# Kernel optimization log

Measured on AMD Instinct MI355X. Metric: run time of the kernel, lower is better.

## Reference

```python
import jax, jax.numpy as jnp
import numpy as np

C_IN = 512
OUT_CH = 256  # query/key gate channels
DIM = 64      # squeeze/extraction rank


def setup_inputs() -> dict:
    key = jax.random.key(0)
    ks = jax.random.split(key, 11)
    b, c, h, w = 16, C_IN, 64, 64

    def winit(k, o, i):
        # torch Conv2d default init: U(-s, s), s = 1/sqrt(fan_in)
        s = 1.0 / np.sqrt(i)
        return jax.random.uniform(k, (o, i), jnp.float32, -s, s)

    return {
        "x": jax.random.normal(ks[0], (b, c, h, w), jnp.float32),
        "Wq": winit(ks[1], OUT_CH, C_IN), "bq": winit(ks[2], OUT_CH, C_IN)[:, 0],
        "Wk": winit(ks[3], OUT_CH, C_IN), "bk": winit(ks[4], OUT_CH, C_IN)[:, 0],
        "Wv": winit(ks[5], C_IN, C_IN),   "bv": winit(ks[6], C_IN, C_IN)[:, 0],
        "Ws": winit(ks[7], DIM, C_IN),    "bs": winit(ks[8], DIM, C_IN)[:, 0],
        "We": winit(ks[9], DIM, C_IN),    "be": winit(ks[10], DIM, C_IN)[:, 0],
    }


def reference(x, Wq, bq, Wk, bk, Wv, bv, Ws, bs, We, be):
    b, c, h, w = x.shape
    n = h * w
    xf = x.reshape(b, c, n)  # [b, 512, n] (1x1 conv == matmul over channels)

    Q = jnp.einsum('oc,bcn->bon', Wq, xf) + bq[:, None]   # [b, 256, n]
    K = jnp.einsum('oc,bcn->bon', Wk, xf) + bk[:, None]   # [b, 256, n]
    gate = jax.nn.sigmoid(jnp.mean(Q * K, axis=1, keepdims=True))  # [b, 1, n]

    V = jnp.einsum('oc,bcn->bon', Wv, xf) + bv[:, None]   # [b, 512, n]
    V_dw = V * gate                                        # [b, 512, n]

    Qs = jnp.einsum('oc,bcn->bon', Ws, xf) + bs[:, None]   # [b, 64, n]
    Ke = jnp.einsum('oc,bcn->bon', We, xf) + be[:, None]   # [b, 64, n]

    energy = jnp.einsum('bcn,bdn->bcd', V_dw, Qs)           # [b, 512, 64]
    attention = jax.nn.softmax(energy, axis=-1)
    Vout = jnp.einsum('bcd,bdn->bcn', attention, Ke)        # [b, 512, n]

    return x + Vout.reshape(b, c, h, w)
```

## Files before the change

### kernel.cpp

```cpp
#include <hip/hip_runtime.h>

#define BATCH 16
#define CIN 512
#define NPIX 4096

typedef __attribute__((ext_vector_type(8))) short bf16x8;
typedef __attribute__((ext_vector_type(4))) float f32x4;

#define MFMA(a,b,c) __builtin_amdgcn_mfma_f32_16x16x32_bf16((a),(b),(c),0,0,0)

union PK  { short s[8]; bf16x8 v; };
union PK4 { short s[4]; uint2 u; };

__device__ __forceinline__ unsigned short bf16_rne(float f){
  unsigned u = __float_as_uint(f);
  return (unsigned short)((u + 0x7fffu + ((u >> 16) & 1u)) >> 16);
}
__device__ __forceinline__ void f32_split(float f, short &h, short &l){
  unsigned short hu = bf16_rne(f);
  h = (short)hu;
  float fh = __uint_as_float((unsigned)hu << 16);
  l = (short)bf16_rne(f - fh);
}
__device__ __forceinline__ void split8(float4 a, float4 b, bf16x8 &h, bf16x8 &l){
  float vv[8] = {a.x,a.y,a.z,a.w,b.x,b.y,b.z,b.w};
  PK ph, pl;
  #pragma unroll
  for (int z=0;z<8;z++){ short hh,ll; f32_split(vv[z],hh,ll); ph.s[z]=hh; pl.s[z]=ll; }
  h = ph.v; l = pl.v;
}

__device__ __forceinline__ int offBig(int row, int k){
  int s = k >> 3;
  s = (s & ~7) | ((s ^ row) & 7);
  return row*512 + s*8 + (k & 7);
}

__global__ __launch_bounds__(256)
void k_convw(const float* __restrict__ Wq, const float* __restrict__ bq,
             const float* __restrict__ Wk, const float* __restrict__ bk,
             const float* __restrict__ Ws, const float* __restrict__ bs,
             const float* __restrict__ We, const float* __restrict__ be,
             short* __restrict__ WG, short* __restrict__ WSE, short* __restrict__ WSL,
             float* __restrict__ BG, float* __restrict__ BSE){
  int t = blockIdx.x*256 + threadIdx.x;
  if (t < 512*512){
    int r = t >> 9, c = t & 511, o = r >> 1;
    float v = (r & 1) ? Wk[o*512+c] : Wq[o*512+c];
    WG[t] = (short)bf16_rne(v);
  }
  if (t < 128*512){
    int r = t >> 9, c = t & 511;
    float v = (r < 64) ? Ws[r*512+c] : We[(r-64)*512+c];
    short h,l; f32_split(v,h,l);
    WSE[t] = h;
    if (r < 64) WSL[t] = l;
  }
  if (t < 512) BG[t] = (t&1) ? bk[t>>1] : bq[t>>1];
  if (t < 128) BSE[t] = (t < 64) ? bs[t] : be[t-64];
}

__global__ __launch_bounds__(512)
void k_front(const float* __restrict__ x, const short* __restrict__ WG,
             const float* __restrict__ BG, const short* __restrict__ WSE,
             const short* __restrict__ WSL, const float* __restrict__ BSE,
             float* __restrict__ QSG, short* __restrict__ KET, float* __restrict__ S){
  __shared__ __align__(16) short XS[64*512];
  __shared__ float QKf[512];
  __shared__ float GF[64];
  int nt = blockIdx.x, b = blockIdx.y;
  int n0 = nt*64;
  int tid = threadIdx.x, w = tid>>6, lane = tid&63;
  int lr = lane&15, lk = (lane>>4)<<3;
  bool isQs = (w < 4);
  const short* wgb = WG  + (size_t)(w*64 + lr)*512 + lk;
  const short* wb  = WSE + (size_t)((isQs ? (w*16) : (64 + (w-4)*16)) + lr)*512 + lk;
  const short* wlb = WSL + (size_t)((isQs ? (w*16) : 0) + lr)*512 + lk;

  {
    const float* xp = x + ((size_t)b*CIN + tid)*NPIX + n0;
    for (int i=0;i<64;i+=4){
      float4 v = *(const float4*)(xp + i);
      float vv[4] = {v.x, v.y, v.z, v.w};
      #pragma unroll
      for (int u=0;u<4;u++)
        XS[offBig(i+u, tid)] = (short)bf16_rne(vv[u]);
    }
  }
  __syncthreads();

  f32x4 acc1[4][4] = {};
  f32x4 acc2[4] = {};

  bf16x8 c0 = *(const bf16x8*)(wgb + 0*16*512);
  bf16x8 c1 = *(const bf16x8*)(wgb + 1*16*512);
  bf16x8 c2 = *(const bf16x8*)(wgb + 2*16*512);
  bf16x8 c3 = *(const bf16x8*)(wgb + 3*16*512);
  bf16x8 chh = *(const bf16x8*)(wb);
  bf16x8 cll = isQs ? *(const bf16x8*)(wlb) : chh;

  for (int kt=0; kt<16; kt++){
    bf16x8 n0f=c0, n1f=c1, n2f=c2, n3f=c3, nhf=chh, nlf=cll;
    if (kt < 15){
      int o = (kt+1)*32;
      n0f = *(const bf16x8*)(wgb + 0*16*512 + o);
      n1f = *(const bf16x8*)(wgb + 1*16*512 + o);
      n2f = *(const bf16x8*)(wgb + 2*16*512 + o);
      n3f = *(const bf16x8*)(wgb + 3*16*512 + o);
      nhf = *(const bf16x8*)(wb + o);
      nlf = isQs ? *(const bf16x8*)(wlb + o) : nhf;
    }
    bf16x8 bb[4];
    #pragma unroll
    for (int j=0;j<4;j++)
      bb[j] = *(const bf16x8*)&XS[offBig(j*16+lr, kt*32+lk)];
    if (isQs){
      #pragma unroll
      for (int j=0;j<4;j++){
        acc2[j] = MFMA(cll, bb[j], acc2[j]);
        acc2[j] = MFMA(chh, bb[j], acc2[j]);
      }
    } else {
      #pragma unroll
      for (int j=0;j<4;j++)
        acc2[j] = MFMA(chh, bb[j], acc2[j]);
    }
    #pragma unroll
    for (int j=0;j<4;j++) acc1[0][j] = MFMA(c0, bb[j], acc1[0][j]);
    #pragma unroll
    for (int j=0;j<4;j++) acc1[1][j] = MFMA(c1, bb[j], acc1[1][j]);
    #pragma unroll
    for (int j=0;j<4;j++) acc1[2][j] = MFMA(c2, bb[j], acc1[2][j]);
    #pragma unroll
    for (int j=0;j<4;j++) acc1[3][j] = MFMA(c3, bb[j], acc1[3][j]);
    c0=n0f; c1=n1f; c2=n2f; c3=n3f; chh=nhf; cll=nlf;
  }

  int rq = (lane>>4)<<2;
  {
    float p[4] = {0.f,0.f,0.f,0.f};
    #pragma unroll
    for (int r=0;r<4;r++){
      f32x4 bg = *(const f32x4*)&BG[w*64 + r*16 + rq];
      #pragma unroll
      for (int j=0;j<4;j++){
        f32x4 a4 = acc1[r][j];
        p[j] += (a4[0]+bg[0])*(a4[1]+bg[1]) + (a4[2]+bg[2])*(a4[3]+bg[3]);
      }
    }
    #pragma unroll
    for (int j=0;j<4;j++){ p[j] += __shfl_xor(p[j],16); p[j] += __shfl_xor(p[j],32); }
    if (lane < 16){
      #pragma unroll
      for (int j=0;j<4;j++) QKf[w*64 + j*16 + lane] = p[j];
    }
  }
  __syncthreads();
  if (tid < 64){
    float s = 0.f;
    #pragma unroll
    for (int ww=0;ww<8;ww++) s += QKf[ww*64 + tid];
    GF[tid] = 1.f/(1.f + __expf(-s*(1.f/256.f)));
  }
  __syncthreads();

  if (isQs){
    int row0 = w*16 + rq;
    f32x4 bs4 = *(const f32x4*)&BSE[row0];
    float srow[4] = {0.f,0.f,0.f,0.f};
    #pragma unroll
    for (int j=0;j<4;j++){
      int nl = j*16 + lr;
      float g = GF[nl];
      int n = n0 + nl;
      #pragma unroll
      for (int q=0;q<4;q++){
        float v = (acc2[j][q] + bs4[q]) * g;
        QSG[((size_t)(b*64) + row0 + q)*NPIX + n] = v;
        srow[q] += v;
      }
    }
    #pragma unroll
    for (int q=0;q<4;q++){
      float v = srow[q];
      v += __shfl_xor(v,1); v += __shfl_xor(v,2);
      v += __shfl_xor(v,4); v += __shfl_xor(v,8);
      if (lr == 0) atomicAdd(&S[b*64 + row0 + q], v);
    }
  } else {
    int d0 = (w-4)*16 + rq;
    f32x4 be4 = *(const f32x4*)&BSE[64 + d0];
    #pragma unroll
    for (int j=0;j<4;j++){
      int n = n0 + j*16 + lr;
      PK4 pk;
      #pragma unroll
      for (int q=0;q<4;q++) pk.s[q] = (short)bf16_rne(acc2[j][q] + be4[q]);
      *(uint2*)&KET[((size_t)(b*NPIX) + n)*64 + d0] = pk.u;
    }
  }
}

__global__ __launch_bounds__(512)
void k_M(const float* __restrict__ x, const float* __restrict__ QSG,
         float* __restrict__ M){
  int slab = blockIdx.x, b = blockIdx.y;
  int tid = threadIdx.x, w = tid>>6, lane = tid&63;
  int lr = lane&15, lk8 = (lane>>4)<<3;
  f32x4 acc[4][4] = {};
  for (int kt=0; kt<4; kt++){
    int noff = slab*128 + kt*32 + lk8;
    bf16x8 bh[4], bl[4];
    #pragma unroll
    for (int j=0;j<4;j++){
      const float* qp = QSG + ((size_t)(b*64) + j*16 + lr)*NPIX + noff;
      split8(*(const float4*)qp, *(const float4*)(qp+4), bh[j], bl[j]);
    }
    #pragma unroll
    for (int r=0;r<4;r++){
      const float* xp = x + ((size_t)(b*CIN) + w*64 + r*16 + lr)*NPIX + noff;
      bf16x8 ah, al;
      split8(*(const float4*)xp, *(const float4*)(xp+4), ah, al);
      #pragma unroll
      for (int j=0;j<4;j++){
        acc[r][j] = MFMA(al, bh[j], acc[r][j]);
        acc[r][j] = MFMA(ah, bl[j], acc[r][j]);
        acc[r][j] = MFMA(ah, bh[j], acc[r][j]);
      }
    }
  }
  int rq = (lane>>4)<<2;
  #pragma unroll
  for (int r=0;r<4;r++)
    #pragma unroll
    for (int j=0;j<4;j++)
      #pragma unroll
      for (int q=0;q<4;q++)
        atomicAdd(&M[((size_t)(b*CIN) + w*64 + r*16 + rq + q)*64 + j*16 + lr], acc[r][j][q]);
}

__global__ __launch_bounds__(256)
void k_energy(const float* __restrict__ Wv, const float* __restrict__ bv,
              const float* __restrict__ M, const float* __restrict__ S,
              float* __restrict__ EN){
  __shared__ __align__(16) float ML[128*68];
  int cch = blockIdx.x, b = blockIdx.y;
  int tid = threadIdx.x;
  int d4 = tid & 15, ci = tid >> 4;
  f32x4 acc[2] = {};
  for (int kt=0; kt<4; kt++){
    __syncthreads();
    for (int i = tid; i < 2048; i += 256){
      int k = i >> 4, c4 = (i & 15) * 4;
      *(float4*)&ML[k*68 + c4] = *(const float4*)&M[((size_t)(b*CIN) + kt*128 + k)*64 + c4];
    }
    __syncthreads();
    #pragma unroll
    for (int m=0;m<2;m++){
      int c = cch*32 + ci + 16*m;
      const float* wvp = Wv + (size_t)c*512 + kt*128;
      for (int k4=0;k4<32;k4++){
        float4 wv4 = *(const float4*)(wvp + k4*4);
        f32x4 m0 = *(const f32x4*)&ML[(k4*4+0)*68 + d4*4];
        f32x4 m1 = *(const f32x4*)&ML[(k4*4+1)*68 + d4*4];
        f32x4 m2 = *(const f32x4*)&ML[(k4*4+2)*68 + d4*4];
        f32x4 m3 = *(const f32x4*)&ML[(k4*4+3)*68 + d4*4];
        acc[m] += m0*wv4.x + m1*wv4.y + m2*wv4.z + m3*wv4.w;
      }
    }
  }
  f32x4 s4 = *(const f32x4*)&S[b*64 + d4*4];
  #pragma unroll
  for (int m=0;m<2;m++){
    int c = cch*32 + ci + 16*m;
    f32x4 r = acc[m] + s4*bv[c];
    *(f32x4*)&EN[((size_t)(b*CIN) + c)*64 + d4*4] = r;
  }
}

__global__ __launch_bounds__(256)
void k_softmax(const float* __restrict__ EN, short* __restrict__ ATT){
  int row = blockIdx.x*4 + (threadIdx.x>>6);
  int lane = threadIdx.x & 63;
  float v = EN[(size_t)row*64 + lane];
  float m = v;
  #pragma unroll
  for (int s=1;s<64;s<<=1) m = fmaxf(m, __shfl_xor(m, s));
  float e = __expf(v - m);
  float sum = e;
  #pragma unroll
  for (int s=1;s<64;s<<=1) sum += __shfl_xor(sum, s);
  ATT[(size_t)row*64 + lane] = (short)bf16_rne(e / sum);
}

__global__ __launch_bounds__(512)
void k_out(const float* __restrict__ x, const short* __restrict__ ATT,
           const short* __restrict__ KET, float* __restrict__ out){
  int nt = blockIdx.x, b = blockIdx.y;
  int n0 = nt*64;
  int tid = threadIdx.x, w = tid>>6, lane = tid&63;
  int lr = lane&15, lk = (lane>>4)<<3;
  f32x4 acc[4][4] = {};
  #pragma unroll
  for (int kt=0; kt<2; kt++){
    bf16x8 bb[4];
    #pragma unroll
    for (int j=0;j<4;j++)
      bb[j] = *(const bf16x8*)&KET[((size_t)(b*NPIX) + n0 + j*16 + lr)*64 + kt*32 + lk];
    #pragma unroll
    for (int r=0;r<4;r++){
      bf16x8 a = *(const bf16x8*)&ATT[((size_t)(b*CIN) + w*64 + r*16 + lr)*64 + kt*32 + lk];
      #pragma unroll
      for (int j=0;j<4;j++)
        acc[r][j] = MFMA(a, bb[j], acc[r][j]);
    }
  }
  int rq = (lane>>4)<<2;
  #pragma unroll
  for (int r=0;r<4;r++)
    #pragma unroll
    for (int j=0;j<4;j++){
      int col = n0 + j*16 + lr;
      #pragma unroll
      for (int q=0;q<4;q++){
        size_t idx = ((size_t)(b*CIN) + w*64 + r*16 + rq + q)*NPIX + col;
        out[idx] = x[idx] + acc[r][j][q];
      }
    }
}

extern "C" void kernel_launch(void* const* d_in, const int* in_sizes, int n_in,
                              void* d_out, int out_size, void* d_ws, size_t ws_size,
                              hipStream_t stream){
  const float* x   = (const float*)d_in[0];
  const float* Wq  = (const float*)d_in[1];
  const float* bq  = (const float*)d_in[2];
  const float* Wk  = (const float*)d_in[3];
  const float* bk  = (const float*)d_in[4];
  const float* Wv  = (const float*)d_in[5];
  const float* bv  = (const float*)d_in[6];
  const float* Wsq = (const float*)d_in[7];
  const float* bsq = (const float*)d_in[8];
  const float* We  = (const float*)d_in[9];
  const float* be  = (const float*)d_in[10];
  float* out = (float*)d_out;

  char* wsb = (char*)d_ws;
  size_t off = 0;
  auto alloc = [&](size_t bytes)->void*{
    void* p = wsb + off; off += (bytes + 255) & ~(size_t)255; return p;
  };
  short* WG   = (short*)alloc((size_t)512*512*2);
  short* WSE  = (short*)alloc((size_t)128*512*2);
  short* WSL  = (short*)alloc((size_t)64*512*2);
  float* BG   = (float*)alloc(512*4);
  float* BSE  = (float*)alloc(128*4);
  float* QSG  = (float*)alloc((size_t)BATCH*64*NPIX*4);
  short* KET  = (short*)alloc((size_t)BATCH*NPIX*64*2);
  float* Mb   = (float*)alloc((size_t)BATCH*512*64*4);
  float* Sb   = (float*)alloc((size_t)BATCH*64*4);
  float* EN   = (float*)alloc((size_t)BATCH*512*64*4);
  short* ATT  = (short*)alloc((size_t)BATCH*512*64*2);

  hipMemsetAsync(Mb, 0, (size_t)BATCH*512*64*4, stream);
  hipMemsetAsync(Sb, 0, (size_t)BATCH*64*4, stream);

  k_convw  <<<1024, 256, 0, stream>>>(Wq,bq,Wk,bk,Wsq,bsq,We,be, WG,WSE,WSL,BG,BSE);
  k_front  <<<dim3(64,16), 512, 0, stream>>>(x, WG, BG, WSE, WSL, BSE, QSG, KET, Sb);
  k_M      <<<dim3(32,16), 512, 0, stream>>>(x, QSG, Mb);
  k_energy <<<dim3(16,16), 256, 0, stream>>>(Wv, bv, Mb, Sb, EN);
  k_softmax<<<2048, 256, 0, stream>>>(EN, ATT);
  k_out    <<<dim3(64,16), 512, 0, stream>>>(x, ATT, KET, out);
}
```

Measured before the change: 305.4 us.

## Widen k_front to 128-pixel tiles with 1024 threads; double k_M slab

k_front now runs 1024-thread blocks covering 128 pixels, with two 8-wave groups sharing one LDS tile of x and the same weight rows, halving the grid. k_M processes 256 pixels per slab instead of 128, halving its grid and its atomic/partial outputs. The aim is better amortisation of weight loads and fewer blocks, at the cost of 128 KB of LDS per block, lower occupancy, and fewer blocks to fill the CUs (512 and 256 blocks).

```diff
diff --git a/kernel.cpp b/kernel.cpp
--- a/kernel.cpp
+++ b/kernel.cpp
@@ -60,31 +60,34 @@
   if (t < 128) BSE[t] = (t < 64) ? bs[t] : be[t-64];
 }
 
-__global__ __launch_bounds__(512)
+__global__ __launch_bounds__(1024)
 void k_front(const float* __restrict__ x, const short* __restrict__ WG,
              const float* __restrict__ BG, const short* __restrict__ WSE,
              const short* __restrict__ WSL, const float* __restrict__ BSE,
              float* __restrict__ QSG, short* __restrict__ KET, float* __restrict__ S){
-  __shared__ __align__(16) short XS[64*512];
-  __shared__ float QKf[512];
-  __shared__ float GF[64];
+  __shared__ __align__(16) short XS[128*512];
+  __shared__ float QKf[1024];
+  __shared__ float GF[128];
   int nt = blockIdx.x, b = blockIdx.y;
-  int n0 = nt*64;
+  int n0 = nt*128;
   int tid = threadIdx.x, w = tid>>6, lane = tid&63;
+  int wl = w & 7, wg = w >> 3;
+  int n0g = n0 + wg*64;
   int lr = lane&15, lk = (lane>>4)<<3;
-  bool isQs = (w < 4);
-  const short* wgb = WG  + (size_t)(w*64 + lr)*512 + lk;
-  const short* wb  = WSE + (size_t)((isQs ? (w*16) : (64 + (w-4)*16)) + lr)*512 + lk;
-  const short* wlb = WSL + (size_t)((isQs ? (w*16) : 0) + lr)*512 + lk;
+  bool isQs = (wl < 4);
+  const short* wgb = WG  + (size_t)(wl*64 + lr)*512 + lk;
+  const short* wb  = WSE + (size_t)((isQs ? (wl*16) : (64 + (wl-4)*16)) + lr)*512 + lk;
+  const short* wlb = WSL + (size_t)((isQs ? (wl*16) : 0) + lr)*512 + lk;
 
   {
-    const float* xp = x + ((size_t)b*CIN + tid)*NPIX + n0;
+    int cl = tid & 511, nh = tid >> 9;
+    const float* xp = x + ((size_t)b*CIN + cl)*NPIX + n0 + nh*64;
     for (int i=0;i<64;i+=4){
       float4 v = *(const float4*)(xp + i);
       float vv[4] = {v.x, v.y, v.z, v.w};
       #pragma unroll
       for (int u=0;u<4;u++)
-        XS[offBig(i+u, tid)] = (short)bf16_rne(vv[u]);
+        XS[offBig(nh*64 + i+u, cl)] = (short)bf16_rne(vv[u]);
     }
   }
   __syncthreads();
@@ -113,7 +116,7 @@
     bf16x8 bb[4];
     #pragma unroll
     for (int j=0;j<4;j++)
-      bb[j] = *(const bf16x8*)&XS[offBig(j*16+lr, kt*32+lk)];
+      bb[j] = *(const bf16x8*)&XS[offBig(wg*64 + j*16 + lr, kt*32 + lk)];
     if (isQs){
       #pragma unroll
       for (int j=0;j<4;j++){
@@ -141,7 +144,7 @@
     float p[4] = {0.f,0.f,0.f,0.f};
     #pragma unroll
     for (int r=0;r<4;r++){
-      f32x4 bg = *(const f32x4*)&BG[w*64 + r*16 + rq];
+      f32x4 bg = *(const f32x4*)&BG[wl*64 + r*16 + rq];
       #pragma unroll
       for (int j=0;j<4;j++){
         f32x4 a4 = acc1[r][j];
@@ -152,27 +155,28 @@
     for (int j=0;j<4;j++){ p[j] += __shfl_xor(p[j],16); p[j] += __shfl_xor(p[j],32); }
     if (lane < 16){
       #pragma unroll
-      for (int j=0;j<4;j++) QKf[w*64 + j*16 + lane] = p[j];
+      for (int j=0;j<4;j++) QKf[wg*512 + wl*64 + j*16 + lane] = p[j];
     }
   }
   __syncthreads();
-  if (tid < 64){
+  if (tid < 128){
+    int h = tid >> 6, nl = tid & 63;
     float s = 0.f;
     #pragma unroll
-    for (int ww=0;ww<8;ww++) s += QKf[ww*64 + tid];
-    GF[tid] = 1.f/(1.f + __expf(-s*(1.f/256.f)));
+    for (int ww=0;ww<8;ww++) s += QKf[h*512 + ww*64 + nl];
+    GF[h*64 + nl] = 1.f/(1.f + __expf(-s*(1.f/256.f)));
   }
   __syncthreads();
 
   if (isQs){
-    int row0 = w*16 + rq;
+    int row0 = wl*16 + rq;
     f32x4 bs4 = *(const f32x4*)&BSE[row0];
     float srow[4] = {0.f,0.f,0.f,0.f};
     #pragma unroll
     for (int j=0;j<4;j++){
       int nl = j*16 + lr;
-      float g = GF[nl];
-      int n = n0 + nl;
+      float g = GF[wg*64 + nl];
+      int n = n0g + nl;
       #pragma unroll
       for (int q=0;q<4;q++){
         float v = (acc2[j][q] + bs4[q]) * g;
@@ -188,11 +192,11 @@
       if (lr == 0) atomicAdd(&S[b*64 + row0 + q], v);
     }
   } else {
-    int d0 = (w-4)*16 + rq;
+    int d0 = (wl-4)*16 + rq;
     f32x4 be4 = *(const f32x4*)&BSE[64 + d0];
     #pragma unroll
     for (int j=0;j<4;j++){
-      int n = n0 + j*16 + lr;
+      int n = n0g + j*16 + lr;
       PK4 pk;
       #pragma unroll
       for (int q=0;q<4;q++) pk.s[q] = (short)bf16_rne(acc2[j][q] + be4[q]);
@@ -208,8 +212,8 @@
   int tid = threadIdx.x, w = tid>>6, lane = tid&63;
   int lr = lane&15, lk8 = (lane>>4)<<3;
   f32x4 acc[4][4] = {};
-  for (int kt=0; kt<4; kt++){
-    int noff = slab*128 + kt*32 + lk8;
+  for (int kt=0; kt<8; kt++){
+    int noff = slab*256 + kt*32 + lk8;
     bf16x8 bh[4], bl[4];
     #pragma unroll
     for (int j=0;j<4;j++){
@@ -366,8 +370,8 @@
   hipMemsetAsync(Sb, 0, (size_t)BATCH*64*4, stream);
 
   k_convw  <<<1024, 256, 0, stream>>>(Wq,bq,Wk,bk,Wsq,bsq,We,be, WG,WSE,WSL,BG,BSE);
-  k_front  <<<dim3(64,16), 512, 0, stream>>>(x, WG, BG, WSE, WSL, BSE, QSG, KET, Sb);
-  k_M      <<<dim3(32,16), 512, 0, stream>>>(x, QSG, Mb);
+  k_front  <<<dim3(32,16), 1024, 0, stream>>>(x, WG, BG, WSE, WSL, BSE, QSG, KET, Sb);
+  k_M      <<<dim3(16,16), 512, 0, stream>>>(x, QSG, Mb);
   k_energy <<<dim3(16,16), 256, 0, stream>>>(Wv, bv, Mb, Sb, EN);
   k_softmax<<<2048, 256, 0, stream>>>(EN, ATT);
   k_out    <<<dim3(64,16), 512, 0, stream>>>(x, ATT, KET, out);
```

New measurement: 477.5 us. 1.56x slower.
